# Optimization experiments

Measured on AMD Instinct MI355X. Metric: run time of the kernel, lower is better.

## Reference

```python
import jax, jax.numpy as jnp
import numpy as np


def setup_inputs() -> dict:
    key = jax.random.key(0)
    k1, k2 = jax.random.split(key)
    B, T, D = 16, 512, 384
    MAX_LEN = 4096
    x = jax.random.normal(k1, (B, T, D), dtype=jnp.float32)
    durations = jax.random.randint(k2, (B, T), 0, 8, dtype=jnp.int64)
    return {"x": x, "durations": durations, "max_len": MAX_LEN}


def reference(x, durations, max_len):
    # x: (B, T, D), durations: (B, T) int
    B, T, D = x.shape
    cum = jnp.cumsum(durations, axis=1)          # (B, T) exclusive-of-nothing cumulative ends
    mel_len = cum[:, -1]                         # (B,) actual (uncapped) frame lengths
    frames = jnp.arange(max_len)                 # (F,)
    # phoneme index owning each output frame: searchsorted on cumulative ends
    idx = jax.vmap(lambda c: jnp.searchsorted(c, frames, side='right'))(cum)  # (B, F)
    idx = jnp.clip(idx, 0, T - 1)
    out = jnp.take_along_axis(x, idx[:, :, None], axis=1)  # (B, F, D)
    # zero-pad frames beyond each item's length (and beyond max_len truncation)
    valid = frames[None, :] < jnp.minimum(mel_len, max_len)[:, None]  # (B, F)
    out = out * valid[:, :, None].astype(out.dtype)
    return out, mel_len
```

## Files before the change

kernel.cpp:

```cpp
#include <hip/hip_runtime.h>


#define B_ 16
#define T_ 512
#define D_ 384
#define MAXLEN_ 4096
#define ROWV4_ (D_ / 4)
#define OUT_ELEMS_ (B_ * MAXLEN_ * D_)

#define FPB_ 64
#define GT_ 384
#define BPB_ (MAXLEN_ / FPB_)
#define KK_ (FPB_ / 4)

typedef float vf4 __attribute__((ext_vector_type(4)));

__global__ __launch_bounds__(T_) void lr_scan_kernel(const int* __restrict__ dur,
                                                     int* __restrict__ cum_ws,
                                                     float* __restrict__ mel_out) {
    const int b = blockIdx.x, t = threadIdx.x;
    const int lane = t & 63, w = t >> 6;
    int v = dur[b * T_ + t];
    #pragma unroll
    for (int off = 1; off < 64; off <<= 1) {
        int n = __shfl_up(v, off);
        if (lane >= off) v += n;
    }
    __shared__ int wsum[8];
    if (lane == 63) wsum[w] = v;
    __syncthreads();
    if (t < 8) {
        int u = wsum[t];
        #pragma unroll
        for (int off = 1; off < 8; off <<= 1) {
            int n = __shfl_up(u, off);
            if (t >= off) u += n;
        }
        wsum[t] = u;
    }
    __syncthreads();
    const int cum = v + (w > 0 ? wsum[w - 1] : 0);
    cum_ws[b * T_ + t] = cum;
    if (t == T_ - 1) mel_out[b] = (float)cum;
}

__global__ __launch_bounds__(GT_) void lr_gather_kernel(const vf4* __restrict__ x,
                                                        const int* __restrict__ cum_ws,
                                                        const int* __restrict__ max_len_p,
                                                        vf4* __restrict__ out) {
    __shared__ int s[T_];
    __shared__ int sidx[FPB_];
    const int t = threadIdx.x;
    const int b = blockIdx.x / BPB_;
    const int f0 = (blockIdx.x - b * BPB_) * FPB_;

    const int lim = min(cum_ws[b * T_ + T_ - 1], max_len_p[0]);

    const int fl = t / 96;
    const int col = t - fl * 96;
    vf4* ob = out + ((size_t)b * MAXLEN_ + f0) * ROWV4_;

    if (f0 >= lim) {
        const vf4 zero = (vf4)(0.f);
        #pragma unroll
        for (int k = 0; k < KK_; ++k)
            ob[(fl + 4 * k) * ROWV4_ + col] = zero;
        return;
    }

    if (t < T_ / 4)
        ((int4*)s)[t] = ((const int4*)(cum_ws + b * T_))[t];
    __syncthreads();

    if (t < FPB_) {
        const int f = f0 + t;
        int idx = -1;
        if (f < lim) {
            idx = 0;
            #pragma unroll
            for (int step = 256; step > 0; step >>= 1)
                if (s[idx + step - 1] <= f) idx += step;
            if (idx > T_ - 1) idx = T_ - 1;
        }
        sidx[t] = idx;
    }
    __syncthreads();

    const vf4* xb = x + (size_t)(b * T_) * ROWV4_;

    int idxr[KK_];
    #pragma unroll
    for (int k = 0; k < KK_; ++k)
        idxr[k] = sidx[fl + 4 * k];

    if (f0 + FPB_ <= lim) {
        vf4 v[KK_];
        #pragma unroll
        for (int k = 0; k < KK_; ++k)
            v[k] = xb[idxr[k] * ROWV4_ + col];
        #pragma unroll
        for (int k = 0; k < KK_; ++k)
            ob[(fl + 4 * k) * ROWV4_ + col] = v[k];
    } else {
        const vf4 zero = (vf4)(0.f);
        vf4 v[KK_];
        #pragma unroll
        for (int k = 0; k < KK_; ++k) {
            v[k] = zero;
            if (idxr[k] >= 0) v[k] = xb[idxr[k] * ROWV4_ + col];
        }
        #pragma unroll
        for (int k = 0; k < KK_; ++k)
            ob[(fl + 4 * k) * ROWV4_ + col] = v[k];
    }
}

extern "C" void kernel_launch(void* const* d_in, const int* in_sizes, int n_in,
                              void* d_out, int out_size, void* d_ws, size_t ws_size,
                              hipStream_t stream) {
    const float* x = (const float*)d_in[0];
    const int* dur = (const int*)d_in[1];
    const int* max_len_p = (const int*)d_in[2];

    float* out = (float*)d_out;
    float* mel_out = out + OUT_ELEMS_;
    int* cum_ws = (int*)d_ws;

    lr_scan_kernel<<<B_, T_, 0, stream>>>(dur, cum_ws, mel_out);

    lr_gather_kernel<<<B_ * BPB_, GT_, 0, stream>>>(
        (const vf4*)x, cum_ws, max_len_p, (vf4*)out);
}
```

Baseline: 122.1 us.

## Fuse duration scan into gather kernel, recomputing cumsum per block

Removes the separate scan kernel and the workspace round trip. Every gather block now loads its batch's 512 durations and computes the prefix sum itself in shared memory, with 256 threads each handling two elements. This saves one kernel launch and the dependency between the two kernels, at the cost of redundant scan work in each of the 1024 blocks. Fully padded blocks now also run the scan before they exit.

```diff
diff --git a/kernel.cpp b/kernel.cpp
--- a/kernel.cpp
+++ b/kernel.cpp
@@ -15,62 +15,63 @@
 
 typedef float vf4 __attribute__((ext_vector_type(4)));
 
-__global__ __launch_bounds__(T_) void lr_scan_kernel(const int* __restrict__ dur,
-                                                     int* __restrict__ cum_ws,
-                                                     float* __restrict__ mel_out) {
-    const int b = blockIdx.x, t = threadIdx.x;
+__global__ __launch_bounds__(GT_) void lr_fused_kernel(const vf4* __restrict__ x,
+                                                       const int* __restrict__ dur,
+                                                       const int* __restrict__ max_len_p,
+                                                       vf4* __restrict__ out,
+                                                       float* __restrict__ mel_out) {
+    __shared__ int s[T_];
+    __shared__ int sidx[FPB_];
+    __shared__ int wsum[4];
+    const int t = threadIdx.x;
+    const int b = blockIdx.x / BPB_;
+    const int f0 = (blockIdx.x - b * BPB_) * FPB_;
+
+    int v = 0, d1 = 0;
     const int lane = t & 63, w = t >> 6;
-    int v = dur[b * T_ + t];
-    #pragma unroll
-    for (int off = 1; off < 64; off <<= 1) {
-        int n = __shfl_up(v, off);
-        if (lane >= off) v += n;
+    if (t < 256) {
+        const int d0 = dur[b * T_ + 2 * t];
+        d1 = dur[b * T_ + 2 * t + 1];
+        v = d0 + d1;
+        #pragma unroll
+        for (int off = 1; off < 64; off <<= 1) {
+            int n = __shfl_up(v, off);
+            if (lane >= off) v += n;
+        }
+        if (lane == 63) wsum[w] = v;
     }
-    __shared__ int wsum[8];
-    if (lane == 63) wsum[w] = v;
     __syncthreads();
-    if (t < 8) {
+    if (t < 4) {
         int u = wsum[t];
         #pragma unroll
-        for (int off = 1; off < 8; off <<= 1) {
+        for (int off = 1; off < 4; off <<= 1) {
             int n = __shfl_up(u, off);
             if (t >= off) u += n;
         }
         wsum[t] = u;
     }
     __syncthreads();
-    const int cum = v + (w > 0 ? wsum[w - 1] : 0);
-    cum_ws[b * T_ + t] = cum;
-    if (t == T_ - 1) mel_out[b] = (float)cum;
-}
+    if (t < 256) {
+        const int cum1 = v + (w > 0 ? wsum[w - 1] : 0);
+        s[2 * t + 1] = cum1;
+        s[2 * t]     = cum1 - d1;
+    }
+    __syncthreads();
 
-__global__ __launch_bounds__(GT_) void lr_gather_kernel(const vf4* __restrict__ x,
-                                                        const int* __restrict__ cum_ws,
-                                                        const int* __restrict__ max_len_p,
-                                                        vf4* __restrict__ out) {
-    __shared__ int s[T_];
-    __shared__ int sidx[FPB_];
-    const int t = threadIdx.x;
-    const int b = blockIdx.x / BPB_;
-    const int f0 = (blockIdx.x - b * BPB_) * FPB_;
+    if (f0 == 0 && t == 0) mel_out[b] = (float)s[T_ - 1];
 
-    const int lim = min(cum_ws[b * T_ + T_ - 1], max_len_p[0]);
-
+    const int lim = min(s[T_ - 1], max_len_p[0]);
     const int fl = t / 96;
     const int col = t - fl * 96;
     vf4* ob = out + ((size_t)b * MAXLEN_ + f0) * ROWV4_;
+    const vf4 zero = (vf4)(0.f);
 
     if (f0 >= lim) {
-        const vf4 zero = (vf4)(0.f);
         #pragma unroll
         for (int k = 0; k < KK_; ++k)
             ob[(fl + 4 * k) * ROWV4_ + col] = zero;
         return;
     }
-
-    if (t < T_ / 4)
-        ((int4*)s)[t] = ((const int4*)(cum_ws + b * T_))[t];
-    __syncthreads();
 
     if (t < FPB_) {
         const int f = f0 + t;
@@ -87,31 +88,29 @@
     __syncthreads();
 
     const vf4* xb = x + (size_t)(b * T_) * ROWV4_;
-
     int idxr[KK_];
     #pragma unroll
     for (int k = 0; k < KK_; ++k)
         idxr[k] = sidx[fl + 4 * k];
 
     if (f0 + FPB_ <= lim) {
-        vf4 v[KK_];
+        vf4 vv[KK_];
         #pragma unroll
         for (int k = 0; k < KK_; ++k)
-            v[k] = xb[idxr[k] * ROWV4_ + col];
+            vv[k] = xb[idxr[k] * ROWV4_ + col];
         #pragma unroll
         for (int k = 0; k < KK_; ++k)
-            ob[(fl + 4 * k) * ROWV4_ + col] = v[k];
+            ob[(fl + 4 * k) * ROWV4_ + col] = vv[k];
     } else {
-        const vf4 zero = (vf4)(0.f);
-        vf4 v[KK_];
+        vf4 vv[KK_];
         #pragma unroll
         for (int k = 0; k < KK_; ++k) {
-            v[k] = zero;
-            if (idxr[k] >= 0) v[k] = xb[idxr[k] * ROWV4_ + col];
+            vv[k] = zero;
+            if (idxr[k] >= 0) vv[k] = xb[idxr[k] * ROWV4_ + col];
         }
         #pragma unroll
         for (int k = 0; k < KK_; ++k)
-            ob[(fl + 4 * k) * ROWV4_ + col] = v[k];
+            ob[(fl + 4 * k) * ROWV4_ + col] = vv[k];
     }
 }
 
@@ -124,10 +123,7 @@
 
     float* out = (float*)d_out;
     float* mel_out = out + OUT_ELEMS_;
-    int* cum_ws = (int*)d_ws;
 
-    lr_scan_kernel<<<B_, T_, 0, stream>>>(dur, cum_ws, mel_out);
-
-    lr_gather_kernel<<<B_ * BPB_, GT_, 0, stream>>>(
-        (const vf4*)x, cum_ws, max_len_p, (vf4*)out);
+    lr_fused_kernel<<<B_ * BPB_, GT_, 0, stream>>>(
+        (const vf4*)x, dur, max_len_p, (vf4*)out, mel_out);
 }
```

Result: no change. 119.9 us (-1.8%).
